# Kernel optimization log

Hardware: AMD Instinct MI355X
Metric: run time of the kernel (lower is better)

## Reference

```python
import jax, jax.numpy as jnp
import numpy as np

D_MODEL = 1024
N_HEADS = 16
HEAD_DIM = D_MODEL // N_HEADS


def setup_inputs() -> dict:
    key = jax.random.key(0)
    k_x, k_q, k_k, k_v = jax.random.split(key, 4)
    B, S = 2, 2048
    x = jax.random.normal(k_x, (B, S, D_MODEL), dtype=jnp.float32)
    # nn.Linear weights stored as [out, in]; we apply x @ W.T
    scale = 1.0 / np.sqrt(D_MODEL)
    W_q = jax.random.uniform(k_q, (D_MODEL, D_MODEL), jnp.float32, -scale, scale)
    W_k = jax.random.uniform(k_k, (D_MODEL, D_MODEL), jnp.float32, -scale, scale)
    W_v = jax.random.uniform(k_v, (D_MODEL, D_MODEL), jnp.float32, -scale, scale)
    return {"x": x, "W_q": W_q, "W_k": W_k, "W_v": W_v}


def reference(x, W_q, W_k, W_v):
    B, S, D = x.shape
    H, Hd = N_HEADS, HEAD_DIM
    # QKV projections (Linear with no bias): x @ W.T
    Q = (x @ W_q.T).reshape(B, S, H, Hd).transpose(0, 2, 1, 3)  # [B,H,S,Hd]
    K = (x @ W_k.T).reshape(B, S, H, Hd).transpose(0, 2, 1, 3)
    V = (x @ W_v.T).reshape(B, S, H, Hd).transpose(0, 2, 1, 3)
    scores = jnp.einsum("bhqd,bhkd->bhqk", Q, K) / jnp.sqrt(jnp.float32(Hd))
    attn = jax.nn.softmax(scores, axis=-1)
    out = jnp.einsum("bhqk,bhkd->bhqd", attn, V)  # [B,H,S,Hd]
    return out.transpose(0, 2, 1, 3).reshape(B, S, H * Hd)
```

## Files before the change

kernel.cpp:

```cpp
#include <hip/hip_runtime.h>
#include <stdint.h>


typedef __bf16 bf16x8 __attribute__((ext_vector_type(8)));
typedef __bf16 bf16x4 __attribute__((ext_vector_type(4)));
typedef __bf16 bf16x2 __attribute__((ext_vector_type(2)));
typedef float  f32x2  __attribute__((ext_vector_type(2)));
typedef float  f32x4  __attribute__((ext_vector_type(4)));
typedef float  f32x16 __attribute__((ext_vector_type(16)));

#define D_MODEL 1024
#define SEQ     2048
#define NHEAD   16
#define HDIM    64
#define BS      4096

__device__ __forceinline__ void load_lds16(const void* g, void* lds) {
  __builtin_amdgcn_global_load_lds(
      (__attribute__((address_space(1))) void*)(uintptr_t)g,
      (__attribute__((address_space(3))) void*)(uintptr_t)lds,
      16, 0, 0);
}

#if __has_builtin(__builtin_amdgcn_exp2f)
#define EXP2F(x) __builtin_amdgcn_exp2f(x)
#else
#define EXP2F(x) __expf(0.6931471805599453f * (x))
#endif

__device__ __forceinline__ uint32_t pack_bf16_pair(float a, float b) {
  f32x2 f = {a, b};
  union { bf16x2 h; uint32_t u; } r;
  r.h = __builtin_convertvector(f, bf16x2);
  return r.u;
}

#define NX4 1048576
#define NW4 262144
__global__ void cvt_all(const float* __restrict__ x,  const float* __restrict__ wq,
                        const float* __restrict__ wk, const float* __restrict__ wv,
                        __bf16* __restrict__ xb,  __bf16* __restrict__ wqb,
                        __bf16* __restrict__ wkb, __bf16* __restrict__ wvb) {
  int i = blockIdx.x * blockDim.x + threadIdx.x;
  const float* in; __bf16* out; int j;
  if (i < NX4)                { in = x;  out = xb;  j = i; }
  else if (i < NX4 + NW4)     { in = wq; out = wqb; j = i - NX4; }
  else if (i < NX4 + 2*NW4)   { in = wk; out = wkb; j = i - NX4 - NW4; }
  else                        { in = wv; out = wvb; j = i - NX4 - 2*NW4; }
  float4 v = ((const float4*)in)[j];
  bf16x4 o;
  o[0] = (__bf16)v.x; o[1] = (__bf16)v.y;
  o[2] = (__bf16)v.z; o[3] = (__bf16)v.w;
  ((bf16x4*)out)[j] = o;
}

__global__ __launch_bounds__(256) void qkv_gemm(
    const __bf16* __restrict__ X,
    const __bf16* __restrict__ Wq, const __bf16* __restrict__ Wk,
    const __bf16* __restrict__ Wv,
    __bf16* __restrict__ Qb, __bf16* __restrict__ Kb, __bf16* __restrict__ Vt) {
  __shared__ __bf16 As[128 * 32];
  __shared__ __bf16 Bs[128 * 32];

  const __bf16* W = (blockIdx.z == 0) ? Wq : (blockIdx.z == 1) ? Wk : Wv;

  const int t    = threadIdx.x;
  const int wv   = t >> 6;
  const int lane = t & 63;
  const int l15  = lane & 15;
  const int quad = lane >> 4;
  const int m0   = blockIdx.y * 128;
  const int n0   = blockIdx.x * 128;
  const int wm   = (wv >> 1) * 64;
  const int wn   = (wv & 1) * 64;

  f32x4 acc[4][4] = {};

  for (int it = 0; it < 32; ++it) {
    const int k0 = it * 32;
#pragma unroll
    for (int p = 0; p < 2; ++p) {
      const int c   = p * 256 + t;
      const int row = c >> 2;
      const int ko  = (c & 3) * 8;
      const unsigned lb = (unsigned)((p * 256 + wv * 64) * 16);
      load_lds16(X + (size_t)(m0 + row) * D_MODEL + k0 + ko, (char*)As + lb);
      load_lds16(W + (size_t)(n0 + row) * D_MODEL + k0 + ko, (char*)Bs + lb);
    }
    __syncthreads();

    bf16x8 af[4], bfb[4];
#pragma unroll
    for (int i = 0; i < 4; ++i)
      af[i] = *(const bf16x8*)&As[(wm + i * 16 + l15) * 32 + quad * 8];
#pragma unroll
    for (int j = 0; j < 4; ++j)
      bfb[j] = *(const bf16x8*)&Bs[(wn + j * 16 + l15) * 32 + quad * 8];
#pragma unroll
    for (int i = 0; i < 4; ++i)
#pragma unroll
      for (int j = 0; j < 4; ++j)
        acc[i][j] = __builtin_amdgcn_mfma_f32_16x16x32_bf16(af[i], bfb[j],
                                                            acc[i][j], 0, 0, 0);
    __syncthreads();
  }

  if (blockIdx.z != 2) {
    __bf16* Out = (blockIdx.z == 0) ? Qb : Kb;
    const float qs = (blockIdx.z == 0) ? 0.125f * 1.4426950408889634f : 1.0f;
#pragma unroll
    for (int i = 0; i < 4; ++i) {
      const int rg = m0 + wm + i * 16 + quad * 4;
#pragma unroll
      for (int j = 0; j < 4; ++j) {
        const int cg = n0 + wn + j * 16 + l15;
#pragma unroll
        for (int r2 = 0; r2 < 4; ++r2)
          Out[(size_t)(rg + r2) * D_MODEL + cg] = (__bf16)(acc[i][j][r2] * qs);
      }
    }
  } else {
#pragma unroll
    for (int i = 0; i < 4; ++i) {
      const int mg = m0 + wm + i * 16 + quad * 4;
#pragma unroll
      for (int j = 0; j < 4; ++j) {
        const int ng = n0 + wn + j * 16 + l15;
        bf16x4 v;
#pragma unroll
        for (int r2 = 0; r2 < 4; ++r2) v[r2] = (__bf16)acc[i][j][r2];
        *(bf16x4*)&Vt[(size_t)ng * BS + mg] = v;
      }
    }
  }
}

__global__ __launch_bounds__(256) void attn(
    const __bf16* __restrict__ Qb, const __bf16* __restrict__ Kb,
    const __bf16* __restrict__ Vt, float* __restrict__ out) {
  __shared__ __align__(16) char smem[16896];
  __bf16* Ks = (__bf16*)smem;
  __bf16* Vs = (__bf16*)(smem + 8192);
  float*  cmb = (float*)smem;

  const int t     = threadIdx.x;
  const int wv    = t >> 6;
  const int qgrp  = wv >> 1;
  const int ktile = wv & 1;
  const int lane  = t & 63;
  const int l31   = lane & 31;
  const int half  = lane >> 5;
  const int h     = blockIdx.y;
  const size_t bo = (size_t)blockIdx.z * SEQ;
  const int q0    = blockIdx.x * 64 + qgrp * 32;
  const int hd0   = h * HDIM;

  bf16x8 qf[4];
#pragma unroll
  for (int c = 0; c < 4; ++c)
    qf[c] = *(const bf16x8*)&Qb[(bo + q0 + l31) * D_MODEL + hd0 + c * 16 + half * 8];

  const int rr = t >> 3;
  const int cc = (t & 7) ^ (rr & 7);
  const __bf16* kp0 = Kb + (bo + rr) * D_MODEL + hd0 + cc * 8;
  const __bf16* kp1 = Kb + (bo + 32 + rr) * D_MODEL + hd0 + cc * 8;
  const __bf16* vp0 = Vt + (size_t)(hd0 + rr) * BS + bo + cc * 8;
  const __bf16* vp1 = Vt + (size_t)(hd0 + 32 + rr) * BS + bo + cc * 8;
  char* const kD0 = (char*)Ks + wv * 1024;
  char* const kD1 = (char*)Ks + 4096 + wv * 1024;
  char* const vD0 = (char*)Vs + wv * 1024;
  char* const vD1 = (char*)Vs + 4096 + wv * 1024;

  const int srow = ktile * 32 + l31;

  unsigned kOff[4];
#pragma unroll
  for (int c = 0; c < 4; ++c) {
    const int pc = (2 * c + half) ^ (srow & 7);
    kOff[c] = (unsigned)((srow * 8 + pc) * 16);
  }
  unsigned vOff[4];
#pragma unroll
  for (int kc = 0; kc < 2; ++kc)
#pragma unroll
    for (int dt = 0; dt < 2; ++dt) {
      const int row = dt * 32 + l31;
      const int pc  = (ktile * 4 + kc * 2 + half) ^ (row & 7);
      vOff[kc * 2 + dt] = (unsigned)((row * 8 + pc) * 16);
    }

  f32x2 lsum2 = {0.f, 0.f};
  f32x16 o_acc[2] = {};

  for (int kt = 0; kt < SEQ / 64; ++kt) {
    load_lds16(kp0, kD0);
    load_lds16(kp1, kD1);
    load_lds16(vp0, vD0);
    load_lds16(vp1, vD1);
    kp0 += 64 * D_MODEL; kp1 += 64 * D_MODEL;
    vp0 += 64;           vp1 += 64;
    __syncthreads();

    f32x16 st = {};
#pragma unroll
    for (int c = 0; c < 4; ++c) {
      bf16x8 kf = *(const bf16x8*)((const char*)Ks + kOff[c]);
      st = __builtin_amdgcn_mfma_f32_32x32x16_bf16(kf, qf[c], st, 0, 0, 0);
    }

    uint32_t pk[8];
#pragma unroll
    for (int i = 0; i < 8; ++i) {
      float e0 = EXP2F(st[2 * i]);
      float e1 = EXP2F(st[2 * i + 1]);
      f32x2 e = {e0, e1};
      lsum2 += e;
      pk[i] = pack_bf16_pair(e0, e1);
    }

#pragma unroll
    for (int kc = 0; kc < 2; ++kc) {
      auto r02 = __builtin_amdgcn_permlane32_swap(pk[kc * 4 + 0], pk[kc * 4 + 2],
                                                  false, false);
      auto r13 = __builtin_amdgcn_permlane32_swap(pk[kc * 4 + 1], pk[kc * 4 + 3],
                                                  false, false);
      union { uint32_t u[4]; bf16x8 v; } pf;
      pf.u[0] = r02[0]; pf.u[1] = r13[0];
      pf.u[2] = r02[1]; pf.u[3] = r13[1];
#pragma unroll
      for (int dt = 0; dt < 2; ++dt) {
        bf16x8 vf = *(const bf16x8*)((const char*)Vs + vOff[kc * 2 + dt]);
        o_acc[dt] = __builtin_amdgcn_mfma_f32_32x32x16_bf16(vf, pf.v,
                                                            o_acc[dt], 0, 0, 0);
      }
    }
    __syncthreads();
  }

  float lsum = lsum2[0] + lsum2[1];

  if (ktile == 1) {
    float* p = cmb + (size_t)(qgrp * 64 + lane) * 33;
#pragma unroll
    for (int dt = 0; dt < 2; ++dt)
#pragma unroll
      for (int g = 0; g < 16; ++g) p[dt * 16 + g] = o_acc[dt][g];
    p[32] = lsum;
  }
  __syncthreads();
  if (ktile == 0) {
    const float* p = cmb + (size_t)(qgrp * 64 + lane) * 33;
#pragma unroll
    for (int dt = 0; dt < 2; ++dt)
#pragma unroll
      for (int g = 0; g < 16; ++g) o_acc[dt][g] += p[dt * 16 + g];
    lsum += p[32];
    lsum += __shfl_xor(lsum, 32);
    const float inv = 1.f / lsum;

    const size_t orow = (bo + q0 + l31) * D_MODEL + hd0;
#pragma unroll
    for (int dt = 0; dt < 2; ++dt)
#pragma unroll
      for (int g = 0; g < 4; ++g) {
        float4 v = make_float4(o_acc[dt][4 * g + 0] * inv, o_acc[dt][4 * g + 1] * inv,
                               o_acc[dt][4 * g + 2] * inv, o_acc[dt][4 * g + 3] * inv);
        *(float4*)&out[orow + dt * 32 + g * 8 + half * 4] = v;
      }
  }
}

extern "C" void kernel_launch(void* const* d_in, const int* in_sizes, int n_in,
                              void* d_out, int out_size, void* d_ws, size_t ws_size,
                              hipStream_t stream) {
  const float* x  = (const float*)d_in[0];
  const float* Wq = (const float*)d_in[1];
  const float* Wk = (const float*)d_in[2];
  const float* Wv = (const float*)d_in[3];
  float* out = (float*)d_out;

  char* ws = (char*)d_ws;
  __bf16* xb  = (__bf16*)(ws);
  __bf16* wqb = (__bf16*)(ws + (8u  << 20));
  __bf16* wkb = (__bf16*)(ws + (10u << 20));
  __bf16* wvb = (__bf16*)(ws + (12u << 20));
  __bf16* Qbf = (__bf16*)(ws + (14u << 20));
  __bf16* Kbf = (__bf16*)(ws + (22u << 20));
  __bf16* Vt  = (__bf16*)(ws + (30u << 20));

  cvt_all<<<(NX4 + 3 * NW4) / 256, 256, 0, stream>>>(x, Wq, Wk, Wv,
                                                     xb, wqb, wkb, wvb);

  qkv_gemm<<<dim3(8, 32, 3), 256, 0, stream>>>(xb, wqb, wkb, wvb, Qbf, Kbf, Vt);

  attn<<<dim3(SEQ / 64, NHEAD, 2), 256, 0, stream>>>(Qbf, Kbf, Vt, out);
}
```

Measured before the change: 162.9 us.

## Process two query tiles per attention block to reuse K/V LDS loads

Each attention block now handles 128 queries, as two 32-row query groups per wave, instead of 64. The K and V fragments are read from LDS into registers once per tile and reused for both query groups. This halves the number of K/V global-to-LDS loads per query and the number of block barriers per unit of work. The costs are higher register pressure from a second set of accumulators and Q fragments, half as many blocks for occupancy (512 total), and a serialized two-pass combine epilogue.

Result: faster. 158.0 us (-3.0%).

```diff
diff --git a/kernel.cpp b/kernel.cpp
--- a/kernel.cpp
+++ b/kernel.cpp
@@ -152,13 +152,16 @@
   const int half  = lane >> 5;
   const int h     = blockIdx.y;
   const size_t bo = (size_t)blockIdx.z * SEQ;
-  const int q0    = blockIdx.x * 64 + qgrp * 32;
+  const int q0A   = blockIdx.x * 128 + qgrp * 32;
+  const int q0B   = q0A + 64;
   const int hd0   = h * HDIM;
 
-  bf16x8 qf[4];
-#pragma unroll
-  for (int c = 0; c < 4; ++c)
-    qf[c] = *(const bf16x8*)&Qb[(bo + q0 + l31) * D_MODEL + hd0 + c * 16 + half * 8];
+  bf16x8 qfA[4], qfB[4];
+#pragma unroll
+  for (int c = 0; c < 4; ++c) {
+    qfA[c] = *(const bf16x8*)&Qb[(bo + q0A + l31) * D_MODEL + hd0 + c * 16 + half * 8];
+    qfB[c] = *(const bf16x8*)&Qb[(bo + q0B + l31) * D_MODEL + hd0 + c * 16 + half * 8];
+  }
 
   const int rr = t >> 3;
   const int cc = (t & 7) ^ (rr & 7);
@@ -189,8 +192,8 @@
       vOff[kc * 2 + dt] = (unsigned)((row * 8 + pc) * 16);
     }
 
-  f32x2 lsum2 = {0.f, 0.f};
-  f32x16 o_acc[2] = {};
+  f32x2 lsum2A = {0.f, 0.f}, lsum2B = {0.f, 0.f};
+  f32x16 o_accA[2] = {}, o_accB[2] = {};
 
   for (int kt = 0; kt < SEQ / 64; ++kt) {
     load_lds16(kp0, kD0);
@@ -201,51 +204,85 @@
     vp0 += 64;           vp1 += 64;
     __syncthreads();
 
-    f32x16 st = {};
-#pragma unroll
-    for (int c = 0; c < 4; ++c) {
-      bf16x8 kf = *(const bf16x8*)((const char*)Ks + kOff[c]);
-      st = __builtin_amdgcn_mfma_f32_32x32x16_bf16(kf, qf[c], st, 0, 0, 0);
-    }
-
-    uint32_t pk[8];
-#pragma unroll
-    for (int i = 0; i < 8; ++i) {
-      float e0 = EXP2F(st[2 * i]);
-      float e1 = EXP2F(st[2 * i + 1]);
-      f32x2 e = {e0, e1};
-      lsum2 += e;
-      pk[i] = pack_bf16_pair(e0, e1);
-    }
-
-#pragma unroll
-    for (int kc = 0; kc < 2; ++kc) {
-      auto r02 = __builtin_amdgcn_permlane32_swap(pk[kc * 4 + 0], pk[kc * 4 + 2],
-                                                  false, false);
-      auto r13 = __builtin_amdgcn_permlane32_swap(pk[kc * 4 + 1], pk[kc * 4 + 3],
-                                                  false, false);
-      union { uint32_t u[4]; bf16x8 v; } pf;
-      pf.u[0] = r02[0]; pf.u[1] = r13[0];
-      pf.u[2] = r02[1]; pf.u[3] = r13[1];
-#pragma unroll
-      for (int dt = 0; dt < 2; ++dt) {
-        bf16x8 vf = *(const bf16x8*)((const char*)Vs + vOff[kc * 2 + dt]);
-        o_acc[dt] = __builtin_amdgcn_mfma_f32_32x32x16_bf16(vf, pf.v,
-                                                            o_acc[dt], 0, 0, 0);
+    bf16x8 kf[4], vfr[4];
+#pragma unroll
+    for (int c = 0; c < 4; ++c)
+      kf[c] = *(const bf16x8*)((const char*)Ks + kOff[c]);
+#pragma unroll
+    for (int j = 0; j < 4; ++j)
+      vfr[j] = *(const bf16x8*)((const char*)Vs + vOff[j]);
+
+    {
+      f32x16 st = {};
+#pragma unroll
+      for (int c = 0; c < 4; ++c)
+        st = __builtin_amdgcn_mfma_f32_32x32x16_bf16(kf[c], qfA[c], st, 0, 0, 0);
+      uint32_t pk[8];
+#pragma unroll
+      for (int i = 0; i < 8; ++i) {
+        float e0 = EXP2F(st[2 * i]);
+        float e1 = EXP2F(st[2 * i + 1]);
+        f32x2 e = {e0, e1};
+        lsum2A += e;
+        pk[i] = pack_bf16_pair(e0, e1);
+      }
+#pragma unroll
+      for (int kc = 0; kc < 2; ++kc) {
+        auto r02 = __builtin_amdgcn_permlane32_swap(pk[kc * 4 + 0], pk[kc * 4 + 2],
+                                                    false, false);
+        auto r13 = __builtin_amdgcn_permlane32_swap(pk[kc * 4 + 1], pk[kc * 4 + 3],
+                                                    false, false);
+        union { uint32_t u[4]; bf16x8 v; } pf;
+        pf.u[0] = r02[0]; pf.u[1] = r13[0];
+        pf.u[2] = r02[1]; pf.u[3] = r13[1];
+#pragma unroll
+        for (int dt = 0; dt < 2; ++dt)
+          o_accA[dt] = __builtin_amdgcn_mfma_f32_32x32x16_bf16(vfr[kc * 2 + dt], pf.v,
+                                                              o_accA[dt], 0, 0, 0);
+      }
+    }
+    {
+      f32x16 st = {};
+#pragma unroll
+      for (int c = 0; c < 4; ++c)
+        st = __builtin_amdgcn_mfma_f32_32x32x16_bf16(kf[c], qfB[c], st, 0, 0, 0);
+      uint32_t pk[8];
+#pragma unroll
+      for (int i = 0; i < 8; ++i) {
+        float e0 = EXP2F(st[2 * i]);
+        float e1 = EXP2F(st[2 * i + 1]);
+        f32x2 e = {e0, e1};
+        lsum2B += e;
+        pk[i] = pack_bf16_pair(e0, e1);
+      }
+#pragma unroll
+      for (int kc = 0; kc < 2; ++kc) {
+        auto r02 = __builtin_amdgcn_permlane32_swap(pk[kc * 4 + 0], pk[kc * 4 + 2],
+                                                    false, false);
+        auto r13 = __builtin_amdgcn_permlane32_swap(pk[kc * 4 + 1], pk[kc * 4 + 3],
+                                                    false, false);
+        union { uint32_t u[4]; bf16x8 v; } pf;
+        pf.u[0] = r02[0]; pf.u[1] = r13[0];
+        pf.u[2] = r02[1]; pf.u[3] = r13[1];
+#pragma unroll
+        for (int dt = 0; dt < 2; ++dt)
+          o_accB[dt] = __builtin_amdgcn_mfma_f32_32x32x16_bf16(vfr[kc * 2 + dt], pf.v,
+                                                              o_accB[dt], 0, 0, 0);
       }
     }
     __syncthreads();
   }
 
-  float lsum = lsum2[0] + lsum2[1];
+  float lsumA = lsum2A[0] + lsum2A[1];
+  float lsumB = lsum2B[0] + lsum2B[1];
 
   if (ktile == 1) {
     float* p = cmb + (size_t)(qgrp * 64 + lane) * 33;
 #pragma unroll
     for (int dt = 0; dt < 2; ++dt)
 #pragma unroll
-      for (int g = 0; g < 16; ++g) p[dt * 16 + g] = o_acc[dt][g];
-    p[32] = lsum;
+      for (int g = 0; g < 16; ++g) p[dt * 16 + g] = o_accA[dt][g];
+    p[32] = lsumA;
   }
   __syncthreads();
   if (ktile == 0) {
@@ -253,18 +290,46 @@
 #pragma unroll
     for (int dt = 0; dt < 2; ++dt)
 #pragma unroll
-      for (int g = 0; g < 16; ++g) o_acc[dt][g] += p[dt * 16 + g];
-    lsum += p[32];
-    lsum += __shfl_xor(lsum, 32);
-    const float inv = 1.f / lsum;
-
-    const size_t orow = (bo + q0 + l31) * D_MODEL + hd0;
+      for (int g = 0; g < 16; ++g) o_accA[dt][g] += p[dt * 16 + g];
+    lsumA += p[32];
+    lsumA += __shfl_xor(lsumA, 32);
+    const float inv = 1.f / lsumA;
+    const size_t orow = (bo + q0A + l31) * D_MODEL + hd0;
 #pragma unroll
     for (int dt = 0; dt < 2; ++dt)
 #pragma unroll
       for (int g = 0; g < 4; ++g) {
-        float4 v = make_float4(o_acc[dt][4 * g + 0] * inv, o_acc[dt][4 * g + 1] * inv,
-                               o_acc[dt][4 * g + 2] * inv, o_acc[dt][4 * g + 3] * inv);
+        float4 v = make_float4(o_accA[dt][4 * g + 0] * inv, o_accA[dt][4 * g + 1] * inv,
+                               o_accA[dt][4 * g + 2] * inv, o_accA[dt][4 * g + 3] * inv);
+        *(float4*)&out[orow + dt * 32 + g * 8 + half * 4] = v;
+      }
+  }
+  __syncthreads();
+  if (ktile == 1) {
+    float* p = cmb + (size_t)(qgrp * 64 + lane) * 33;
+#pragma unroll
+    for (int dt = 0; dt < 2; ++dt)
+#pragma unroll
+      for (int g = 0; g < 16; ++g) p[dt * 16 + g] = o_accB[dt][g];
+    p[32] = lsumB;
+  }
+  __syncthreads();
+  if (ktile == 0) {
+    const float* p = cmb + (size_t)(qgrp * 64 + lane) * 33;
+#pragma unroll
+    for (int dt = 0; dt < 2; ++dt)
+#pragma unroll
+      for (int g = 0; g < 16; ++g) o_accB[dt][g] += p[dt * 16 + g];
+    lsumB += p[32];
+    lsumB += __shfl_xor(lsumB, 32);
+    const float inv = 1.f / lsumB;
+    const size_t orow = (bo + q0B + l31) * D_MODEL + hd0;
+#pragma unroll
+    for (int dt = 0; dt < 2; ++dt)
+#pragma unroll
+      for (int g = 0; g < 4; ++g) {
+        float4 v = make_float4(o_accB[dt][4 * g + 0] * inv, o_accB[dt][4 * g + 1] * inv,
+                               o_accB[dt][4 * g + 2] * inv, o_accB[dt][4 * g + 3] * inv);
         *(float4*)&out[orow + dt * 32 + g * 8 + half * 4] = v;
       }
   }
@@ -293,5 +358,5 @@
 
   qkv_gemm<<<dim3(8, 32, 3), 256, 0, stream>>>(xb, wqb, wkb, wvb, Qbf, Kbf, Vt);
 
-  attn<<<dim3(SEQ / 64, NHEAD, 2), 256, 0, stream>>>(Qbf, Kbf, Vt, out);
-}
+  attn<<<dim3(SEQ / 128, NHEAD, 2), 256, 0, stream>>>(Qbf, Kbf, Vt, out);
+}
```

## Triple-buffer K/V tiles in LDS with async prefetch and vmcnt-based barriers

Applied to the files above, without the earlier changes.

Replaces the single-buffered load-sync-compute loop in the attention kernel with a three-stage LDS ring buffer. The next tiles are issued via global_load_lds while the current one is computed, and s_waitcnt vmcnt(4) plus a barrier wait only for the older stage. This is meant to hide global memory latency behind the MFMA work. LDS use grows from about 17KB to 48KB per block, which may reduce occupancy, and the manual waitcnt counting depends on exactly four loads per stage.

Result: no change. 160.4 us (-1.6%).

```diff
diff --git a/kernel.cpp b/kernel.cpp
--- a/kernel.cpp
+++ b/kernel.cpp
@@ -34,6 +34,17 @@
   r.h = __builtin_convertvector(f, bf16x2);
   return r.u;
 }
+
+#define WAITBAR4 do {                                      \
+    asm volatile("s_waitcnt vmcnt(4)" ::: "memory");       \
+    __builtin_amdgcn_s_barrier();                          \
+    asm volatile("" ::: "memory");                         \
+  } while (0)
+#define WAITBAR0 do {                                      \
+    asm volatile("s_waitcnt vmcnt(0)" ::: "memory");       \
+    __builtin_amdgcn_s_barrier();                          \
+    asm volatile("" ::: "memory");                         \
+  } while (0)
 
 #define NX4 1048576
 #define NW4 262144
@@ -138,10 +149,8 @@
 __global__ __launch_bounds__(256) void attn(
     const __bf16* __restrict__ Qb, const __bf16* __restrict__ Kb,
     const __bf16* __restrict__ Vt, float* __restrict__ out) {
-  __shared__ __align__(16) char smem[16896];
-  __bf16* Ks = (__bf16*)smem;
-  __bf16* Vs = (__bf16*)(smem + 8192);
-  float*  cmb = (float*)smem;
+  __shared__ __align__(16) char smem[49152];
+  float* cmb = (float*)smem;
 
   const int t     = threadIdx.x;
   const int wv    = t >> 6;
@@ -166,10 +175,23 @@
   const __bf16* kp1 = Kb + (bo + 32 + rr) * D_MODEL + hd0 + cc * 8;
   const __bf16* vp0 = Vt + (size_t)(hd0 + rr) * BS + bo + cc * 8;
   const __bf16* vp1 = Vt + (size_t)(hd0 + 32 + rr) * BS + bo + cc * 8;
-  char* const kD0 = (char*)Ks + wv * 1024;
-  char* const kD1 = (char*)Ks + 4096 + wv * 1024;
-  char* const vD0 = (char*)Vs + wv * 1024;
-  char* const vD1 = (char*)Vs + 4096 + wv * 1024;
+
+  char* const bufA = smem;
+  char* const bufB = smem + 16384;
+  char* const bufC = smem + 32768;
+  const unsigned kd0 = (unsigned)(wv * 1024);
+  const unsigned kd1 = (unsigned)(4096 + wv * 1024);
+  const unsigned vd0 = (unsigned)(8192 + wv * 1024);
+  const unsigned vd1 = (unsigned)(12288 + wv * 1024);
+
+  auto STAGE = [&](char* buf) {
+    load_lds16(kp0, buf + kd0);
+    load_lds16(kp1, buf + kd1);
+    load_lds16(vp0, buf + vd0);
+    load_lds16(vp1, buf + vd1);
+    kp0 += 64 * D_MODEL; kp1 += 64 * D_MODEL;
+    vp0 += 64;           vp1 += 64;
+  };
 
   const int srow = ktile * 32 + l31;
 
@@ -186,25 +208,17 @@
     for (int dt = 0; dt < 2; ++dt) {
       const int row = dt * 32 + l31;
       const int pc  = (ktile * 4 + kc * 2 + half) ^ (row & 7);
-      vOff[kc * 2 + dt] = (unsigned)((row * 8 + pc) * 16);
+      vOff[kc * 2 + dt] = (unsigned)(8192 + (row * 8 + pc) * 16);
     }
 
   f32x2 lsum2 = {0.f, 0.f};
   f32x16 o_acc[2] = {};
 
-  for (int kt = 0; kt < SEQ / 64; ++kt) {
-    load_lds16(kp0, kD0);
-    load_lds16(kp1, kD1);
-    load_lds16(vp0, vD0);
-    load_lds16(vp1, vD1);
-    kp0 += 64 * D_MODEL; kp1 += 64 * D_MODEL;
-    vp0 += 64;           vp1 += 64;
-    __syncthreads();
-
+  auto COMPUTE = [&](const char* base) {
     f32x16 st = {};
 #pragma unroll
     for (int c = 0; c < 4; ++c) {
-      bf16x8 kf = *(const bf16x8*)((const char*)Ks + kOff[c]);
+      bf16x8 kf = *(const bf16x8*)(base + kOff[c]);
       st = __builtin_amdgcn_mfma_f32_32x32x16_bf16(kf, qf[c], st, 0, 0, 0);
     }
 
@@ -229,13 +243,33 @@
       pf.u[2] = r02[1]; pf.u[3] = r13[1];
 #pragma unroll
       for (int dt = 0; dt < 2; ++dt) {
-        bf16x8 vf = *(const bf16x8*)((const char*)Vs + vOff[kc * 2 + dt]);
+        bf16x8 vf = *(const bf16x8*)(base + vOff[kc * 2 + dt]);
         o_acc[dt] = __builtin_amdgcn_mfma_f32_32x32x16_bf16(vf, pf.v,
                                                             o_acc[dt], 0, 0, 0);
       }
     }
-    __syncthreads();
-  }
+  };
+
+  STAGE(bufA);
+  STAGE(bufB);
+  WAITBAR4;
+
+  for (int it = 0; it < 10; ++it) {
+    STAGE(bufC);
+    COMPUTE(bufA);
+    WAITBAR4;
+    STAGE(bufA);
+    COMPUTE(bufB);
+    WAITBAR4;
+    STAGE(bufB);
+    COMPUTE(bufC);
+    WAITBAR4;
+  }
+
+  COMPUTE(bufA);
+  WAITBAR0;
+  COMPUTE(bufB);
+  __syncthreads();
 
   float lsum = lsum2[0] + lsum2[1];
 
```
